# Kernel optimization log

Hardware: AMD Instinct MI355X
Metric: run time of the kernel (lower is better)

The kernel has to match this reference:

```python
import jax, jax.numpy as jnp
import numpy as np

TEMPERATURE = 0.5
NEG_INF = -1e30  # mask value for diagonal in logsumexp (exact -inf also fine)


def _l2norm(x, eps=1e-12):
    # matches F.normalize(dim=1)
    n = jnp.sqrt(jnp.sum(x * x, axis=1, keepdims=True))
    return x / jnp.maximum(n, eps)


def setup_inputs() -> dict:
    key = jax.random.key(0)
    k1, k2, k3 = jax.random.split(key, 3)
    B, D, Q = 2048, 512, 32768
    return {
        "z_i": jax.random.normal(k1, (B, D), dtype=jnp.float32),
        "z_j": jax.random.normal(k2, (B, D), dtype=jnp.float32),
        "queue": jax.random.normal(k3, (Q, D), dtype=jnp.float32),
    }


def reference(z_i, z_j, queue):
    z = jnp.concatenate([z_i, z_j], axis=0)          # [N, D]
    N = z.shape[0]
    features = _l2norm(z)                            # [N, D]
    queue_norm = _l2norm(queue)                      # [Q, D]

    # NN retrieval from the support set
    sims_q = jnp.matmul(features, queue_norm.T)      # [N, Q]
    nn_idx = jnp.argmax(sims_q, axis=1)              # [N]
    nn_feats = queue_norm[nn_idx]                    # [N, D]

    # contrastive similarity between NNs and features
    sim = jnp.matmul(nn_feats, features.T) / TEMPERATURE  # [N, N]

    # positives: off-diagonals at +/- N//2
    sim_i_j = jnp.diagonal(sim, offset=N // 2)       # [N/2]
    sim_j_i = jnp.diagonal(sim, offset=-(N // 2))    # [N/2]
    positive_samples = jnp.concatenate([sim_i_j, sim_j_i], axis=0)  # [N]

    # negatives: all off-diagonal entries per row -> logsumexp with diag masked
    diag_mask = jnp.eye(N, dtype=bool)
    sim_masked = jnp.where(diag_mask, NEG_INF, sim)
    repulsion = jnp.mean(jax.scipy.special.logsumexp(sim_masked, axis=1))

    attraction = -jnp.mean(positive_samples)
    return attraction + repulsion
```

## Files before the change

kernel.cpp:

```cpp
#include <hip/hip_runtime.h>
#include <cstdint>

#define NFEAT 4096
#define NHALF 2048
#define DDIM  512
#define QROWS 32768

typedef unsigned short u16;
typedef unsigned char  u8;
typedef unsigned int   u32;
typedef unsigned long long u64;

typedef float  f32x16_t __attribute__((ext_vector_type(16)));
typedef int    i32x4_t  __attribute__((ext_vector_type(4)));
typedef int    i32x8_t  __attribute__((ext_vector_type(8)));

typedef const __attribute__((address_space(1))) void* gas_ptr;
typedef __attribute__((address_space(3))) void* las_ptr;

__device__ __forceinline__ u32 fkey(float f) {
  u32 u = __float_as_uint(f);
  return (u & 0x80000000u) ? ~u : (u | 0x80000000u);
}

__global__ void k_norm(const float* __restrict__ zi, const float* __restrict__ zj,
                       const float* __restrict__ queue,
                       u8* __restrict__ feat8T, u8* __restrict__ queue8T) {
  int gw = (int)((blockIdx.x * blockDim.x + threadIdx.x) >> 6);
  int lane = threadIdx.x & 63;
  const float* src; u8* dstT; int r31;
  if (gw < NFEAT) {
    src = (gw < NHALF) ? (zi + (size_t)gw * DDIM) : (zj + (size_t)(gw - NHALF) * DDIM);
    dstT = feat8T + (size_t)(gw >> 5) * 16384; r31 = gw & 31;
  } else {
    int r = gw - NFEAT;
    src = queue + (size_t)r * DDIM;
    dstT = queue8T + (size_t)(r >> 5) * 16384; r31 = r & 31;
  }
  float4 v0 = reinterpret_cast<const float4*>(src)[lane * 2];
  float4 v1 = reinterpret_cast<const float4*>(src)[lane * 2 + 1];
  float ss = v0.x*v0.x + v0.y*v0.y + v0.z*v0.z + v0.w*v0.w
           + v1.x*v1.x + v1.y*v1.y + v1.z*v1.z + v1.w*v1.w;
  #pragma unroll
  for (int off = 32; off >= 1; off >>= 1) ss += __shfl_xor(ss, off);
  float inv = 1.0f / fmaxf(sqrtf(ss), 1e-12f);
  float n0 = v0.x*inv, n1 = v0.y*inv, n2 = v0.z*inv, n3 = v0.w*inv;
  float n4 = v1.x*inv, n5 = v1.y*inv, n6 = v1.z*inv, n7 = v1.w*inv;
  u32 p01, p23, p45, p67;
  asm("v_cvt_pk_fp8_f32 %0, %1, %2" : "=v"(p01) : "v"(n0), "v"(n1));
  asm("v_cvt_pk_fp8_f32 %0, %1, %2" : "=v"(p23) : "v"(n2), "v"(n3));
  asm("v_cvt_pk_fp8_f32 %0, %1, %2" : "=v"(p45) : "v"(n4), "v"(n5));
  asm("v_cvt_pk_fp8_f32 %0, %1, %2" : "=v"(p67) : "v"(n6), "v"(n7));
  uint2 w8;
  w8.x = (p01 & 0xFFFFu) | (p23 << 16);
  w8.y = (p45 & 0xFFFFu) | (p67 << 16);
  size_t toff = (size_t)(lane >> 3) * 2048 + ((lane >> 2) & 1) * 1024
              + ((lane >> 1) & 1) * 512 + r31 * 16 + (lane & 1) * 8;
  *reinterpret_cast<uint2*>(dstT + toff) = w8;
}

#define SB0() __builtin_amdgcn_sched_barrier(0)
#define LGKM0_SB() do { asm volatile("s_waitcnt lgkmcnt(0)" ::: "memory"); SB0(); } while (0)
#define VMCNT4() asm volatile("s_waitcnt vmcnt(4)" ::: "memory")
#define VMCNT0() asm volatile("s_waitcnt vmcnt(0)" ::: "memory")
#define SBAR() __builtin_amdgcn_s_barrier()
#define RD(dst, base, off) asm volatile("ds_read_b128 %0, %1 offset:" off \
                                        : "=v"(dst) : "v"(base))
#define MFMA8(ACC, AV, BV) \
  ACC = __builtin_amdgcn_mfma_scale_f32_32x32x64_f8f6f4(AV, BV, ACC, 0, 0, 0, \
        0x7F7F7F7F, 0, 0x7F7F7F7F)

__global__ __launch_bounds__(256, 2) void k_argmax_gemm8(
    const u8* __restrict__ feat8T, const u8* __restrict__ queue8T,
    u64* __restrict__ part) {
  __shared__ u8 lds[49152];
  const int tid = threadIdx.x;
  const int w = tid >> 6, lane = tid & 63;
  const int wr = w >> 1, wc = w & 1;
  const int l31 = lane & 31, hi = lane >> 5;
  const int bid = (int)blockIdx.x;
  const int wg = (bid & 7) * 512 + (bid >> 3);
  const int mt = wg >> 4, ft = wg & 15;
  const int brow = mt * 128, bcol = ft * 256;

  const u8* pA = queue8T + (size_t)(brow >> 5) * 16384 + (tid >> 7) * 16384 + (tid & 127) * 16;
  const u8* pB = feat8T  + (size_t)(bcol >> 5) * 16384 + (tid >> 7) * 16384 + (tid & 127) * 16;
  const u32 dA = (u32)(size_t)(las_ptr)&lds[tid * 16];
  const u32 dB = dA + 8192;

  const u32 aAd = (u32)(size_t)(las_ptr)&lds[wr * 4096 + hi * 1024 + l31 * 16];
  const u32 bAd = (u32)(size_t)(las_ptr)&lds[8192 + wc * 8192 + hi * 1024 + l31 * 16];

  f32x16_t acc00 = {}, acc01 = {}, acc02 = {}, acc03 = {};
  f32x16_t acc10 = {}, acc11 = {}, acc12 = {}, acc13 = {};

  auto stage = [&](int b, int t) {
    const u32 base = (u32)(b * 24576);
    __builtin_amdgcn_global_load_lds((gas_ptr)(pA + t * 2048),         (las_ptr)(size_t)(dA + base), 16, 0, 0);
    __builtin_amdgcn_global_load_lds((gas_ptr)(pA + 32768 + t * 2048), (las_ptr)(size_t)(dA + base + 4096), 16, 0, 0);
    __builtin_amdgcn_global_load_lds((gas_ptr)(pB + t * 2048),         (las_ptr)(size_t)(dB + base), 16, 0, 0);
    __builtin_amdgcn_global_load_lds((gas_ptr)(pB + 32768 + t * 2048), (las_ptr)(size_t)(dB + base + 4096), 16, 0, 0);
    __builtin_amdgcn_global_load_lds((gas_ptr)(pB + 65536 + t * 2048), (las_ptr)(size_t)(dB + base + 8192), 16, 0, 0);
    __builtin_amdgcn_global_load_lds((gas_ptr)(pB + 98304 + t * 2048), (las_ptr)(size_t)(dB + base + 12288), 16, 0, 0);
  };

  stage(0, 0);
  VMCNT0();
  SBAR();

  #pragma unroll
  for (int t = 0; t < 8; t++) {
    if (t < 7) stage((t + 1) & 1, t + 1);
    const u32 bb = (u32)((t & 1) * 24576);
    const u32 xa = aAd + bb, xb = bAd + bb;
    i32x4_t r0, r1, r2, r3, s0, s1, s2, s3, s4, s5, s6, s7;
    RD(r0, xa, "0");    RD(r1, xa, "512");
    RD(r2, xa, "2048"); RD(r3, xa, "2560");
    RD(s0, xb, "0");    RD(s1, xb, "512");
    RD(s2, xb, "2048"); RD(s3, xb, "2560");
    RD(s4, xb, "4096"); RD(s5, xb, "4608");
    RD(s6, xb, "6144"); RD(s7, xb, "6656");
    LGKM0_SB();
    i32x8_t A0 = __builtin_shufflevector(r0, r1, 0, 1, 2, 3, 4, 5, 6, 7);
    i32x8_t A1 = __builtin_shufflevector(r2, r3, 0, 1, 2, 3, 4, 5, 6, 7);
    i32x8_t B0 = __builtin_shufflevector(s0, s1, 0, 1, 2, 3, 4, 5, 6, 7);
    i32x8_t B1 = __builtin_shufflevector(s2, s3, 0, 1, 2, 3, 4, 5, 6, 7);
    i32x8_t B2 = __builtin_shufflevector(s4, s5, 0, 1, 2, 3, 4, 5, 6, 7);
    i32x8_t B3 = __builtin_shufflevector(s6, s7, 0, 1, 2, 3, 4, 5, 6, 7);
    __builtin_amdgcn_s_setprio(1);
    MFMA8(acc00, A0, B0); MFMA8(acc01, A0, B1);
    MFMA8(acc02, A0, B2); MFMA8(acc03, A0, B3);
    MFMA8(acc10, A1, B0); MFMA8(acc11, A1, B1);
    MFMA8(acc12, A1, B2); MFMA8(acc13, A1, B3);
    __builtin_amdgcn_s_setprio(0);
    if (t < 7) { VMCNT0(); SBAR(); }
  }

  const int mslot = mt * 2 + wr;
#define AMAX_N(ACC0, ACC1, NOFF) do { \
    float bv = -3.0e38f; int br = 0; \
    _Pragma("unroll") \
    for (int reg = 0; reg < 16; reg++) { \
      float v = ACC0[reg]; int lr = (reg & 3) + 8 * (reg >> 2); \
      if (v > bv) { bv = v; br = lr; } } \
    _Pragma("unroll") \
    for (int reg = 0; reg < 16; reg++) { \
      float v = ACC1[reg]; int lr = 32 + (reg & 3) + 8 * (reg >> 2); \
      if (v > bv) { bv = v; br = lr; } } \
    u32 q = (u32)(brow + wr * 64 + br + 4 * hi); \
    u64 key = ((u64)fkey(bv) << 32) | (u64)(0xFFFFFFFFu - q); \
    u64 o = __shfl_xor(key, 32); \
    key = key > o ? key : o; \
    int j = bcol + wc * 128 + NOFF + l31; \
    if (hi == 0) part[(size_t)j * 512 + mslot] = key; \
  } while (0)
  AMAX_N(acc00, acc10, 0);
  AMAX_N(acc01, acc11, 32);
  AMAX_N(acc02, acc12, 64);
  AMAX_N(acc03, acc13, 96);
#undef AMAX_N
}

__global__ void k_reduce_gather(const u64* __restrict__ part,
                                const u8* __restrict__ queue8T,
                                u8* __restrict__ nn8T) {
  int row = (int)((blockIdx.x * blockDim.x + threadIdx.x) >> 6);
  int lane = threadIdx.x & 63;
  const u64* p = part + (size_t)row * 512;
  u64 best = 0;
  #pragma unroll
  for (int i = 0; i < 8; i++) { u64 v = p[lane * 8 + i]; best = best > v ? best : v; }
  #pragma unroll
  for (int off = 1; off < 64; off <<= 1) { u64 o = __shfl_xor(best, off); best = best > o ? best : o; }
  int g = (int)(0xFFFFFFFFu - (u32)(best & 0xFFFFFFFFu));
  if (lane < 32) {
    const uint4 v = *reinterpret_cast<const uint4*>(
        queue8T + (size_t)(g >> 5) * 16384 + lane * 512 + (g & 31) * 16);
    *reinterpret_cast<uint4*>(
        nn8T + (size_t)(row >> 5) * 16384 + lane * 512 + (row & 31) * 16) = v;
  }
}

#define FP8_TILE(XA, XB) do { \
    i32x4_t a00, a01, a10, a11, b00, b01, b10, b11; \
    RD(a00, XA, "0"); RD(a01, XA, "512"); \
    RD(a10, XA, "2048"); RD(a11, XA, "2560"); \
    RD(b00, XB, "0"); RD(b01, XB, "512"); \
    RD(b10, XB, "2048"); RD(b11, XB, "2560"); \
    LGKM0_SB(); \
    i32x8_t A0 = __builtin_shufflevector(a00, a01, 0, 1, 2, 3, 4, 5, 6, 7); \
    i32x8_t A1 = __builtin_shufflevector(a10, a11, 0, 1, 2, 3, 4, 5, 6, 7); \
    i32x8_t B0 = __builtin_shufflevector(b00, b01, 0, 1, 2, 3, 4, 5, 6, 7); \
    i32x8_t B1 = __builtin_shufflevector(b10, b11, 0, 1, 2, 3, 4, 5, 6, 7); \
    __builtin_amdgcn_s_setprio(1); \
    MFMA8(acc00, A0, B0); \
    MFMA8(acc01, A0, B1); \
    MFMA8(acc10, A1, B0); \
    MFMA8(acc11, A1, B1); \
    __builtin_amdgcn_s_setprio(0); \
  } while (0)

#define FP8_MAIN_LOOP() do { \
  stage(0, 0); stage(1, 1); \
  VMCNT4(); \
  SBAR(); \
  _Pragma("unroll") \
  for (int t = 0; t < 8; t++) { \
    if (t <= 5) stage((t + 2) % 3, t + 2); \
    const u32 bb = (u32)((t % 3) * 16384); \
    FP8_TILE(aAd + bb, bAd + bb); \
    if (t < 7) { \
      if (t <= 5) VMCNT4(); else VMCNT0(); \
      SBAR(); \
    } \
  } } while (0)

__global__ __launch_bounds__(256, 2) void k_sim_gemm8(
    const u8* __restrict__ feat8T, const u8* __restrict__ nn8T,
    float2* __restrict__ lsep, float* __restrict__ pos) {
  __shared__ u8 lds[49152];
  const int tid = threadIdx.x;
  const int w = tid >> 6, lane = tid & 63;
  const int wr = w >> 1, wc = w & 1;
  const int l31 = lane & 31, hi = lane >> 5;
  const int bid = (int)blockIdx.x;
  const int wg = (bid & 7) * 128 + (bid >> 3);
  const int mt = wg >> 5, nt = wg & 31;
  const int mtb = mt * 128, ntb = nt * 128;

  const u8* pA = feat8T + (size_t)(mtb >> 5) * 16384 + (tid >> 7) * 16384 + (tid & 127) * 16;
  const u8* pB = nn8T   + (size_t)(ntb >> 5) * 16384 + (tid >> 7) * 16384 + (tid & 127) * 16;
  const u32 dA = (u32)(size_t)(las_ptr)&lds[tid * 16];
  const u32 dB = dA + 8192;

  const u32 aAd = (u32)(size_t)(las_ptr)&lds[wr * 4096 + hi * 1024 + l31 * 16];
  const u32 bAd = (u32)(size_t)(las_ptr)&lds[8192 + wc * 4096 + hi * 1024 + l31 * 16];

  f32x16_t acc00 = {}, acc01 = {}, acc10 = {}, acc11 = {};

  auto stage = [&](int b, int t) {
    const u32 base = (u32)(b * 16384);
    __builtin_amdgcn_global_load_lds((gas_ptr)(pA + t * 2048),         (las_ptr)(size_t)(dA + base), 16, 0, 0);
    __builtin_amdgcn_global_load_lds((gas_ptr)(pA + 32768 + t * 2048), (las_ptr)(size_t)(dA + base + 4096), 16, 0, 0);
    __builtin_amdgcn_global_load_lds((gas_ptr)(pB + t * 2048),         (las_ptr)(size_t)(dB + base), 16, 0, 0);
    __builtin_amdgcn_global_load_lds((gas_ptr)(pB + 32768 + t * 2048), (las_ptr)(size_t)(dB + base + 4096), 16, 0, 0);
  };

  FP8_MAIN_LOOP();

  const int mslot = mt * 2 + wr;
  const int ibase = mtb + wr * 64 + 4 * hi;
  #pragma unroll
  for (int n = 0; n < 2; n++) {
    const int j = ntb + wc * 64 + n * 32 + l31;
    const int jp = j ^ NHALF;
    float mx = -3.0e38f;
    #pragma unroll
    for (int m = 0; m < 2; m++) {
      #pragma unroll
      for (int reg = 0; reg < 16; reg++) {
        float v = (n == 0 ? (m == 0 ? acc00[reg] : acc10[reg])
                          : (m == 0 ? acc01[reg] : acc11[reg])) * 2.0f;
        int i = ibase + m * 32 + (reg & 3) + 8 * (reg >> 2);
        if (i == jp) pos[j] = v;
        if (i == j) v = -1.0e30f;
        mx = fmaxf(mx, v);
      }
    }
    float sm = 0.f;
    #pragma unroll
    for (int m = 0; m < 2; m++) {
      #pragma unroll
      for (int reg = 0; reg < 16; reg++) {
        float v = (n == 0 ? (m == 0 ? acc00[reg] : acc10[reg])
                          : (m == 0 ? acc01[reg] : acc11[reg])) * 2.0f;
        int i = ibase + m * 32 + (reg & 3) + 8 * (reg >> 2);
        if (i == j) v = -1.0e30f;
        sm += __expf(v - mx);
      }
    }
    float mo = __shfl_xor(mx, 32);
    float so = __shfl_xor(sm, 32);
    float M = fmaxf(mx, mo);
    sm = sm * __expf(mx - M) + so * __expf(mo - M);
    if (hi == 0) lsep[(size_t)j * 64 + mslot] = make_float2(M, sm);
  }
}

__global__ void k_lse(const float2* __restrict__ lsep, float* __restrict__ lse) {
  int row = (int)((blockIdx.x * blockDim.x + threadIdx.x) >> 6);
  int lane = threadIdx.x & 63;
  float2 p = lsep[(size_t)row * 64 + lane];
  float m = p.x, s = p.y;
  #pragma unroll
  for (int off = 1; off < 64; off <<= 1) {
    float mo = __shfl_xor(m, off), so = __shfl_xor(s, off);
    float M = fmaxf(m, mo);
    s = s * __expf(m - M) + so * __expf(mo - M);
    m = M;
  }
  if (lane == 0) lse[row] = m + __logf(s);
}

__global__ void k_final(const float* __restrict__ lse, const float* __restrict__ pos,
                        float* __restrict__ out) {
  __shared__ float red[4];
  int tid = threadIdx.x;
  float a = 0.f;
  for (int i = tid; i < NFEAT; i += 256) a += lse[i] - pos[i];
  #pragma unroll
  for (int off = 32; off >= 1; off >>= 1) a += __shfl_xor(a, off);
  if ((tid & 63) == 0) red[tid >> 6] = a;
  __syncthreads();
  if (tid == 0) out[0] = (red[0] + red[1] + red[2] + red[3]) / (float)NFEAT;
}

extern "C" void kernel_launch(void* const* d_in, const int* in_sizes, int n_in,
                              void* d_out, int out_size, void* d_ws, size_t ws_size,
                              hipStream_t stream) {
  const float* zi    = (const float*)d_in[0];
  const float* zj    = (const float*)d_in[1];
  const float* queue = (const float*)d_in[2];
  float* out = (float*)d_out;
  char* ws = (char*)d_ws;

  u8*     queue8T = (u8*)(ws + 0);
  u8*     feat8T  = (u8*)(ws + 16777216);
  u8*     nn8T    = (u8*)(ws + 18874368);
  u64*    part    = (u64*)(ws + 20971520);
  float2* lsep    = (float2*)(ws + 37748736);
  float*  pos     = (float*)(ws + 39845888);
  float*  lse     = (float*)(ws + 39862272);

  k_norm<<<9216, 256, 0, stream>>>(zi, zj, queue, feat8T, queue8T);
  k_argmax_gemm8<<<4096, 256, 0, stream>>>(feat8T, queue8T, part);
  k_reduce_gather<<<1024, 256, 0, stream>>>(part, queue8T, nn8T);
  k_sim_gemm8<<<1024, 256, 0, stream>>>(feat8T, nn8T, lsep, pos);
  k_lse<<<1024, 256, 0, stream>>>(lsep, lse);
  k_final<<<1, 256, 0, stream>>>(lse, pos, out);
}
```

Measured before the change: 109.5 us.

## Load B operand directly from global into registers, widen block to 8 waves

The argmax GEMM now runs 8 waves per block, each computing a 64x64 sub-tile instead of 64x128. Only the A (queue) tile is staged through LDS; each wave reads its B (feature) fragments straight from global memory into registers. This shrinks LDS to 16KB and halves the accumulators per wave so more waves fit per CU. In exchange, B reuse through LDS is lost and each wave issues uncached-pattern global loads, with the global load latency now sitting directly in front of the MFMAs.

```diff
diff --git a/kernel.cpp b/kernel.cpp
--- a/kernel.cpp
+++ b/kernel.cpp
@@ -70,68 +70,59 @@
   ACC = __builtin_amdgcn_mfma_scale_f32_32x32x64_f8f6f4(AV, BV, ACC, 0, 0, 0, \
         0x7F7F7F7F, 0, 0x7F7F7F7F)
 
-__global__ __launch_bounds__(256, 2) void k_argmax_gemm8(
+__global__ __launch_bounds__(512, 3) void k_argmax_gemm8(
     const u8* __restrict__ feat8T, const u8* __restrict__ queue8T,
     u64* __restrict__ part) {
-  __shared__ u8 lds[49152];
+  __shared__ u8 lds[16384];
   const int tid = threadIdx.x;
   const int w = tid >> 6, lane = tid & 63;
-  const int wr = w >> 1, wc = w & 1;
+  const int wr = w >> 2, wc = w & 3;
   const int l31 = lane & 31, hi = lane >> 5;
   const int bid = (int)blockIdx.x;
   const int wg = (bid & 7) * 512 + (bid >> 3);
   const int mt = wg >> 4, ft = wg & 15;
   const int brow = mt * 128, bcol = ft * 256;
 
-  const u8* pA = queue8T + (size_t)(brow >> 5) * 16384 + (tid >> 7) * 16384 + (tid & 127) * 16;
-  const u8* pB = feat8T  + (size_t)(bcol >> 5) * 16384 + (tid >> 7) * 16384 + (tid & 127) * 16;
+  const u8* pA = queue8T + (size_t)((brow >> 5) + (tid >> 7)) * 16384 + (tid & 127) * 16;
   const u32 dA = (u32)(size_t)(las_ptr)&lds[tid * 16];
-  const u32 dB = dA + 8192;
 
   const u32 aAd = (u32)(size_t)(las_ptr)&lds[wr * 4096 + hi * 1024 + l31 * 16];
-  const u32 bAd = (u32)(size_t)(las_ptr)&lds[8192 + wc * 8192 + hi * 1024 + l31 * 16];
-
-  f32x16_t acc00 = {}, acc01 = {}, acc02 = {}, acc03 = {};
-  f32x16_t acc10 = {}, acc11 = {}, acc12 = {}, acc13 = {};
-
-  auto stage = [&](int b, int t) {
-    const u32 base = (u32)(b * 24576);
-    __builtin_amdgcn_global_load_lds((gas_ptr)(pA + t * 2048),         (las_ptr)(size_t)(dA + base), 16, 0, 0);
-    __builtin_amdgcn_global_load_lds((gas_ptr)(pA + 32768 + t * 2048), (las_ptr)(size_t)(dA + base + 4096), 16, 0, 0);
-    __builtin_amdgcn_global_load_lds((gas_ptr)(pB + t * 2048),         (las_ptr)(size_t)(dB + base), 16, 0, 0);
-    __builtin_amdgcn_global_load_lds((gas_ptr)(pB + 32768 + t * 2048), (las_ptr)(size_t)(dB + base + 4096), 16, 0, 0);
-    __builtin_amdgcn_global_load_lds((gas_ptr)(pB + 65536 + t * 2048), (las_ptr)(size_t)(dB + base + 8192), 16, 0, 0);
-    __builtin_amdgcn_global_load_lds((gas_ptr)(pB + 98304 + t * 2048), (las_ptr)(size_t)(dB + base + 12288), 16, 0, 0);
+
+  const u8* pB0 = feat8T + (size_t)((bcol >> 5) + wc * 2) * 16384 + hi * 1024 + l31 * 16;
+  const u8* pB1 = pB0 + 16384;
+
+  f32x16_t acc00 = {}, acc01 = {}, acc10 = {}, acc11 = {};
+
+  auto stageA = [&](int b, int t) {
+    __builtin_amdgcn_global_load_lds((gas_ptr)(pA + t * 2048),
+        (las_ptr)(size_t)(dA + (u32)(b * 8192)), 16, 0, 0);
   };
 
-  stage(0, 0);
+  stageA(0, 0);
   VMCNT0();
   SBAR();
 
   #pragma unroll
   for (int t = 0; t < 8; t++) {
-    if (t < 7) stage((t + 1) & 1, t + 1);
-    const u32 bb = (u32)((t & 1) * 24576);
-    const u32 xa = aAd + bb, xb = bAd + bb;
-    i32x4_t r0, r1, r2, r3, s0, s1, s2, s3, s4, s5, s6, s7;
-    RD(r0, xa, "0");    RD(r1, xa, "512");
-    RD(r2, xa, "2048"); RD(r3, xa, "2560");
-    RD(s0, xb, "0");    RD(s1, xb, "512");
-    RD(s2, xb, "2048"); RD(s3, xb, "2560");
-    RD(s4, xb, "4096"); RD(s5, xb, "4608");
-    RD(s6, xb, "6144"); RD(s7, xb, "6656");
+    const u8* q0 = pB0 + t * 2048;
+    const u8* q1 = pB1 + t * 2048;
+    i32x4_t b0l = *reinterpret_cast<const i32x4_t*>(q0);
+    i32x4_t b0h = *reinterpret_cast<const i32x4_t*>(q0 + 512);
+    i32x4_t b1l = *reinterpret_cast<const i32x4_t*>(q1);
+    i32x4_t b1h = *reinterpret_cast<const i32x4_t*>(q1 + 512);
+    if (t < 7) stageA((t + 1) & 1, t + 1);
+    const u32 xa = aAd + (u32)((t & 1) * 8192);
+    i32x4_t a0l, a0h, a1l, a1h;
+    RD(a0l, xa, "0");    RD(a0h, xa, "512");
+    RD(a1l, xa, "2048"); RD(a1h, xa, "2560");
     LGKM0_SB();
-    i32x8_t A0 = __builtin_shufflevector(r0, r1, 0, 1, 2, 3, 4, 5, 6, 7);
-    i32x8_t A1 = __builtin_shufflevector(r2, r3, 0, 1, 2, 3, 4, 5, 6, 7);
-    i32x8_t B0 = __builtin_shufflevector(s0, s1, 0, 1, 2, 3, 4, 5, 6, 7);
-    i32x8_t B1 = __builtin_shufflevector(s2, s3, 0, 1, 2, 3, 4, 5, 6, 7);
-    i32x8_t B2 = __builtin_shufflevector(s4, s5, 0, 1, 2, 3, 4, 5, 6, 7);
-    i32x8_t B3 = __builtin_shufflevector(s6, s7, 0, 1, 2, 3, 4, 5, 6, 7);
+    i32x8_t A0 = __builtin_shufflevector(a0l, a0h, 0, 1, 2, 3, 4, 5, 6, 7);
+    i32x8_t A1 = __builtin_shufflevector(a1l, a1h, 0, 1, 2, 3, 4, 5, 6, 7);
+    i32x8_t B0 = __builtin_shufflevector(b0l, b0h, 0, 1, 2, 3, 4, 5, 6, 7);
+    i32x8_t B1 = __builtin_shufflevector(b1l, b1h, 0, 1, 2, 3, 4, 5, 6, 7);
     __builtin_amdgcn_s_setprio(1);
     MFMA8(acc00, A0, B0); MFMA8(acc01, A0, B1);
-    MFMA8(acc02, A0, B2); MFMA8(acc03, A0, B3);
     MFMA8(acc10, A1, B0); MFMA8(acc11, A1, B1);
-    MFMA8(acc12, A1, B2); MFMA8(acc13, A1, B3);
     __builtin_amdgcn_s_setprio(0);
     if (t < 7) { VMCNT0(); SBAR(); }
   }
@@ -151,13 +142,11 @@
     u64 key = ((u64)fkey(bv) << 32) | (u64)(0xFFFFFFFFu - q); \
     u64 o = __shfl_xor(key, 32); \
     key = key > o ? key : o; \
-    int j = bcol + wc * 128 + NOFF + l31; \
+    int j = bcol + wc * 64 + NOFF + l31; \
     if (hi == 0) part[(size_t)j * 512 + mslot] = key; \
   } while (0)
   AMAX_N(acc00, acc10, 0);
   AMAX_N(acc01, acc11, 32);
-  AMAX_N(acc02, acc12, 64);
-  AMAX_N(acc03, acc13, 96);
 #undef AMAX_N
 }
 
@@ -333,7 +322,7 @@
   float*  lse     = (float*)(ws + 39862272);
 
   k_norm<<<9216, 256, 0, stream>>>(zi, zj, queue, feat8T, queue8T);
-  k_argmax_gemm8<<<4096, 256, 0, stream>>>(feat8T, queue8T, part);
+  k_argmax_gemm8<<<4096, 512, 0, stream>>>(feat8T, queue8T, part);
   k_reduce_gather<<<1024, 256, 0, stream>>>(part, queue8T, nn8T);
   k_sim_gemm8<<<1024, 256, 0, stream>>>(feat8T, nn8T, lsep, pos);
   k_lse<<<1024, 256, 0, stream>>>(lsep, lse);
```

Result: no change. 109.4 us (-0.1%).

## Load GEMM operands directly from global into registers, bypassing LDS staging

Applied to the files above, without the earlier changes.

The fp8 argmax GEMM now loads each wave's A and B fragments straight from global memory into registers with a two-set register double buffer, replacing the global_load_lds staging, LDS reads and block barriers. This removes the LDS round trip and the per-iteration s_barrier and vmcnt(0) waits. In exchange, operand tiles shared between waves are fetched redundantly from global/L2 and register pressure rises, which could limit occupancy at 2 blocks per CU.

```diff
diff --git a/kernel.cpp b/kernel.cpp
--- a/kernel.cpp
+++ b/kernel.cpp
@@ -70,10 +70,32 @@
   ACC = __builtin_amdgcn_mfma_scale_f32_32x32x64_f8f6f4(AV, BV, ACC, 0, 0, 0, \
         0x7F7F7F7F, 0, 0x7F7F7F7F)
 
+#define LD16(dst, p) dst = *reinterpret_cast<const i32x4_t*>(p)
+#define DIRECT_LOAD(S, t) do { \
+    LD16(S##a0l, pA0 + (t) * 2048); LD16(S##a0h, pA0 + (t) * 2048 + 512); \
+    LD16(S##a1l, pA1 + (t) * 2048); LD16(S##a1h, pA1 + (t) * 2048 + 512); \
+    LD16(S##b0l, pB0 + (t) * 2048); LD16(S##b0h, pB0 + (t) * 2048 + 512); \
+    LD16(S##b1l, pB1 + (t) * 2048); LD16(S##b1h, pB1 + (t) * 2048 + 512); \
+    LD16(S##b2l, pB2 + (t) * 2048); LD16(S##b2h, pB2 + (t) * 2048 + 512); \
+    LD16(S##b3l, pB3 + (t) * 2048); LD16(S##b3h, pB3 + (t) * 2048 + 512); } while (0)
+
+#define DO_MFMA(S) do { \
+    i32x8_t A0 = __builtin_shufflevector(S##a0l, S##a0h, 0, 1, 2, 3, 4, 5, 6, 7); \
+    i32x8_t A1 = __builtin_shufflevector(S##a1l, S##a1h, 0, 1, 2, 3, 4, 5, 6, 7); \
+    i32x8_t B0 = __builtin_shufflevector(S##b0l, S##b0h, 0, 1, 2, 3, 4, 5, 6, 7); \
+    i32x8_t B1 = __builtin_shufflevector(S##b1l, S##b1h, 0, 1, 2, 3, 4, 5, 6, 7); \
+    i32x8_t B2 = __builtin_shufflevector(S##b2l, S##b2h, 0, 1, 2, 3, 4, 5, 6, 7); \
+    i32x8_t B3 = __builtin_shufflevector(S##b3l, S##b3h, 0, 1, 2, 3, 4, 5, 6, 7); \
+    __builtin_amdgcn_s_setprio(1); \
+    MFMA8(acc00, A0, B0); MFMA8(acc01, A0, B1); \
+    MFMA8(acc02, A0, B2); MFMA8(acc03, A0, B3); \
+    MFMA8(acc10, A1, B0); MFMA8(acc11, A1, B1); \
+    MFMA8(acc12, A1, B2); MFMA8(acc13, A1, B3); \
+    __builtin_amdgcn_s_setprio(0); } while (0)
+
 __global__ __launch_bounds__(256, 2) void k_argmax_gemm8(
     const u8* __restrict__ feat8T, const u8* __restrict__ queue8T,
     u64* __restrict__ part) {
-  __shared__ u8 lds[49152];
   const int tid = threadIdx.x;
   const int w = tid >> 6, lane = tid & 63;
   const int wr = w >> 1, wc = w & 1;
@@ -83,57 +105,32 @@
   const int mt = wg >> 4, ft = wg & 15;
   const int brow = mt * 128, bcol = ft * 256;
 
-  const u8* pA = queue8T + (size_t)(brow >> 5) * 16384 + (tid >> 7) * 16384 + (tid & 127) * 16;
-  const u8* pB = feat8T  + (size_t)(bcol >> 5) * 16384 + (tid >> 7) * 16384 + (tid & 127) * 16;
-  const u32 dA = (u32)(size_t)(las_ptr)&lds[tid * 16];
-  const u32 dB = dA + 8192;
-
-  const u32 aAd = (u32)(size_t)(las_ptr)&lds[wr * 4096 + hi * 1024 + l31 * 16];
-  const u32 bAd = (u32)(size_t)(las_ptr)&lds[8192 + wc * 8192 + hi * 1024 + l31 * 16];
+  const int lo = hi * 1024 + l31 * 16;
+  const u8* pA0 = queue8T + (size_t)((brow >> 5) + wr * 2) * 16384 + lo;
+  const u8* pA1 = pA0 + 16384;
+  const u8* pB0 = feat8T + (size_t)((bcol >> 5) + wc * 4) * 16384 + lo;
+  const u8* pB1 = pB0 + 16384;
+  const u8* pB2 = pB0 + 32768;
+  const u8* pB3 = pB0 + 49152;
 
   f32x16_t acc00 = {}, acc01 = {}, acc02 = {}, acc03 = {};
   f32x16_t acc10 = {}, acc11 = {}, acc12 = {}, acc13 = {};
 
-  auto stage = [&](int b, int t) {
-    const u32 base = (u32)(b * 24576);
-    __builtin_amdgcn_global_load_lds((gas_ptr)(pA + t * 2048),         (las_ptr)(size_t)(dA + base), 16, 0, 0);
-    __builtin_amdgcn_global_load_lds((gas_ptr)(pA + 32768 + t * 2048), (las_ptr)(size_t)(dA + base + 4096), 16, 0, 0);
-    __builtin_amdgcn_global_load_lds((gas_ptr)(pB + t * 2048),         (las_ptr)(size_t)(dB + base), 16, 0, 0);
-    __builtin_amdgcn_global_load_lds((gas_ptr)(pB + 32768 + t * 2048), (las_ptr)(size_t)(dB + base + 4096), 16, 0, 0);
-    __builtin_amdgcn_global_load_lds((gas_ptr)(pB + 65536 + t * 2048), (las_ptr)(size_t)(dB + base + 8192), 16, 0, 0);
-    __builtin_amdgcn_global_load_lds((gas_ptr)(pB + 98304 + t * 2048), (las_ptr)(size_t)(dB + base + 12288), 16, 0, 0);
-  };
-
-  stage(0, 0);
-  VMCNT0();
-  SBAR();
-
+  i32x4_t p_a0l, p_a0h, p_a1l, p_a1h, p_b0l, p_b0h, p_b1l, p_b1h,
+          p_b2l, p_b2h, p_b3l, p_b3h;
+  i32x4_t q_a0l, q_a0h, q_a1l, q_a1h, q_b0l, q_b0h, q_b1l, q_b1h,
+          q_b2l, q_b2h, q_b3l, q_b3h;
+
+  DIRECT_LOAD(p_, 0);
   #pragma unroll
   for (int t = 0; t < 8; t++) {
-    if (t < 7) stage((t + 1) & 1, t + 1);
-    const u32 bb = (u32)((t & 1) * 24576);
-    const u32 xa = aAd + bb, xb = bAd + bb;
-    i32x4_t r0, r1, r2, r3, s0, s1, s2, s3, s4, s5, s6, s7;
-    RD(r0, xa, "0");    RD(r1, xa, "512");
-    RD(r2, xa, "2048"); RD(r3, xa, "2560");
-    RD(s0, xb, "0");    RD(s1, xb, "512");
-    RD(s2, xb, "2048"); RD(s3, xb, "2560");
-    RD(s4, xb, "4096"); RD(s5, xb, "4608");
-    RD(s6, xb, "6144"); RD(s7, xb, "6656");
-    LGKM0_SB();
-    i32x8_t A0 = __builtin_shufflevector(r0, r1, 0, 1, 2, 3, 4, 5, 6, 7);
-    i32x8_t A1 = __builtin_shufflevector(r2, r3, 0, 1, 2, 3, 4, 5, 6, 7);
-    i32x8_t B0 = __builtin_shufflevector(s0, s1, 0, 1, 2, 3, 4, 5, 6, 7);
-    i32x8_t B1 = __builtin_shufflevector(s2, s3, 0, 1, 2, 3, 4, 5, 6, 7);
-    i32x8_t B2 = __builtin_shufflevector(s4, s5, 0, 1, 2, 3, 4, 5, 6, 7);
-    i32x8_t B3 = __builtin_shufflevector(s6, s7, 0, 1, 2, 3, 4, 5, 6, 7);
-    __builtin_amdgcn_s_setprio(1);
-    MFMA8(acc00, A0, B0); MFMA8(acc01, A0, B1);
-    MFMA8(acc02, A0, B2); MFMA8(acc03, A0, B3);
-    MFMA8(acc10, A1, B0); MFMA8(acc11, A1, B1);
-    MFMA8(acc12, A1, B2); MFMA8(acc13, A1, B3);
-    __builtin_amdgcn_s_setprio(0);
-    if (t < 7) { VMCNT0(); SBAR(); }
+    if ((t & 1) == 0) {
+      if (t < 7) DIRECT_LOAD(q_, t + 1);
+      DO_MFMA(p_);
+    } else {
+      if (t < 7) DIRECT_LOAD(p_, t + 1);
+      DO_MFMA(q_);
+    }
   }
 
   const int mslot = mt * 2 + wr;
```

Measured after the change: 113.4 us. 1.04x slower.
